# Kernel tuning notes

Hardware: AMD Instinct MI355X
Metric: run time of the kernel (lower is better)

## Reference

```python
import jax, jax.numpy as jnp
import numpy as np

B, C, H, W = 32, 1024, 32, 32  # N = H*W must equal C for the attn_c * attn_s broadcast
C8 = C // 8


def setup_inputs() -> dict:
    key = jax.random.key(0)
    ks = jax.random.split(key, 9)
    s = 1.0 / np.sqrt(C)
    return {
        "z": jax.random.normal(ks[0], (B, C, H, W), jnp.float32),
        "x": jax.random.normal(ks[1], (B, C, H, W), jnp.float32),
        "y": jax.random.normal(ks[2], (B, C, H, W), jnp.float32),
        "Wq": jax.random.normal(ks[3], (C8, C), jnp.float32) * s,
        "bq": jax.random.normal(ks[4], (C8,), jnp.float32) * 0.01,
        "Wk": jax.random.normal(ks[5], (C8, C), jnp.float32) * s,
        "bk": jax.random.normal(ks[6], (C8,), jnp.float32) * 0.01,
        "Wv": jax.random.normal(ks[7], (C, C), jnp.float32) * s,
        "bv": jax.random.normal(ks[8], (C,), jnp.float32) * 0.01,
    }


def reference(z, x, y, Wq, bq, Wk, bk, Wv, bv):
    b, c, h, w = x.shape
    n = h * w
    xf = x.reshape(b, c, n)
    yf = y.reshape(b, c, n)
    zf = z.reshape(b, c, n)

    # 1x1 convs == channel matmuls
    q = jnp.einsum('oc,bcn->bon', Wq, xf) + bq[None, :, None]   # (B, C/8, N)
    k = jnp.einsum('oc,bcn->bon', Wk, yf) + bk[None, :, None]   # (B, C/8, N)

    # channel-projected spatial attention: (B, N, N)
    energy_c = jnp.einsum('bcn,bcm->bnm', q, k)
    attention_c = jax.nn.softmax(energy_c, axis=-1)

    # raw channel attention: (B, C, C)
    energy_s = jnp.einsum('bcn,bdn->bcd', xf, yf)
    energy_s = jnp.max(energy_s, axis=-1, keepdims=True) - energy_s
    attention_s = jax.nn.softmax(energy_s, axis=-1)

    # multiplicative combine + third softmax (requires N == C)
    attention = jax.nn.softmax(attention_c * attention_s, axis=-1)

    v = jnp.einsum('oc,bcn->bon', Wv, zf) + bv[None, :, None]   # (B, C, N)
    # out[b,c,m] = sum_n v[b,c,n] * attention[b,m,n]  (value @ attention^T)
    out = jnp.einsum('bcn,bmn->bcm', v, attention)
    return z + out.reshape(b, c, h, w)
```

## Files before the change

kernel.cpp:

```cpp
#include <hip/hip_runtime.h>
#include <hip/hip_bf16.h>

typedef __attribute__((ext_vector_type(8))) short s8_t;
typedef __attribute__((ext_vector_type(4))) float f4_t;

__device__ __forceinline__ unsigned short f2bf(float f) {
  union { float f; unsigned u; } x; x.f = f;
  unsigned r = x.u + 0x7fffu + ((x.u >> 16) & 1u);
  return (unsigned short)(r >> 16);
}

__device__ __forceinline__ void split2(float e0, float e1, unsigned& hp, unsigned& lp) {
  unsigned b0 = __float_as_uint(e0), b1 = __float_as_uint(e1);
  unsigned h0 = b0 & 0xFFFF0000u, h1 = b1 & 0xFFFF0000u;
  hp = (b0 >> 16) | h1;
  float l0 = e0 - __uint_as_float(h0), l1 = e1 - __uint_as_float(h1);
  lp = (__float_as_uint(l0) >> 16) | (__float_as_uint(l1) & 0xFFFF0000u);
}

__device__ __forceinline__ void gload16(const void* g, void* l) {
  __builtin_amdgcn_global_load_lds(
      (const __attribute__((address_space(1))) void*)g,
      (__attribute__((address_space(3))) void*)l, 16, 0, 0);
}

__device__ __forceinline__ void swz_grid(int& bx, int& by, int& bz) {
  const int gx = gridDim.x, gy = gridDim.y;
  const int nwg = gx * gy * gridDim.z;
  const int flat = (blockIdx.z * gy + blockIdx.y) * gx + blockIdx.x;
  const int s = (flat & 7) * (nwg >> 3) + (flat >> 3);
  bx = s % gx;
  const int r = s / gx;
  by = r % gy;
  bz = r / gy;
}

__global__ __launch_bounds__(256) void k_convert(const float* __restrict__ in,
                                                 unsigned short* __restrict__ out, int n) {
  int i = (blockIdx.x * 256 + threadIdx.x) * 8;
  if (i >= n) return;
  float4 a = *(const float4*)(in + i);
  float4 b = *(const float4*)(in + i + 4);
  ushort4 u0; u0.x = f2bf(a.x); u0.y = f2bf(a.y); u0.z = f2bf(a.z); u0.w = f2bf(a.w);
  ushort4 u1; u1.x = f2bf(b.x); u1.y = f2bf(b.y); u1.z = f2bf(b.z); u1.w = f2bf(b.w);
  *(ushort4*)(out + i) = u0;
  *(ushort4*)(out + i + 4) = u1;
}

__global__ __launch_bounds__(256) void k_transp32(const float* __restrict__ in,
                                                  float* __restrict__ out) {
  __shared__ float tile[64][65];
  const int t = threadIdx.x, b = blockIdx.z;
  const int r0 = blockIdx.y * 64, c0 = blockIdx.x * 64;
  const float* ip = in + (size_t)b * 1048576;
  float* op = out + (size_t)b * 1048576;
  const int tr = t >> 4, tc = (t & 15) * 4;
#pragma unroll
  for (int p = 0; p < 4; ++p) {
    int r = p * 16 + tr;
    float4 v = *(const float4*)(ip + (size_t)(r0 + r) * 1024 + c0 + tc);
    tile[r][tc] = v.x; tile[r][tc + 1] = v.y; tile[r][tc + 2] = v.z; tile[r][tc + 3] = v.w;
  }
  __syncthreads();
#pragma unroll
  for (int p = 0; p < 4; ++p) {
    int n = p * 16 + tr;
    float4 w;
    w.x = tile[tc][n]; w.y = tile[tc + 1][n]; w.z = tile[tc + 2][n]; w.w = tile[tc + 3][n];
    *(float4*)(op + (size_t)(c0 + n) * 1024 + r0 + tc) = w;
  }
}

__global__ __launch_bounds__(256) void k_transpbf(const float* __restrict__ in,
                                                  unsigned short* __restrict__ outt) {
  __shared__ unsigned short tile[64][72];
  const int t = threadIdx.x, b = blockIdx.z;
  const int r0 = blockIdx.y * 64, c0 = blockIdx.x * 64;
  const float* ip = in + (size_t)b * 1048576;
  const int tr = t >> 4, tc = (t & 15) * 4;
#pragma unroll
  for (int p = 0; p < 4; ++p) {
    int r = p * 16 + tr;
    float4 v = *(const float4*)(ip + (size_t)(r0 + r) * 1024 + c0 + tc);
    tile[r][tc] = f2bf(v.x); tile[r][tc + 1] = f2bf(v.y);
    tile[r][tc + 2] = f2bf(v.z); tile[r][tc + 3] = f2bf(v.w);
  }
  __syncthreads();
#pragma unroll
  for (int p = 0; p < 4; ++p) {
    int n = p * 16 + tr;
    ushort4 w;
    w.x = tile[tc][n]; w.y = tile[tc + 1][n]; w.z = tile[tc + 2][n]; w.w = tile[tc + 3][n];
    *(ushort4*)(outt + (size_t)b * 1048576 + (size_t)(c0 + n) * 1024 + r0 + tc) = w;
  }
}

__device__ __forceinline__ void split_write(unsigned short* buf, int wbase,
                                            const float* av, const float* bv) {
  unsigned ah[8], al[8], bh[8], bl[8];
#pragma unroll
  for (int p = 0; p < 8; ++p) {
    split2(av[2 * p], av[2 * p + 1], ah[p], al[p]);
    split2(bv[2 * p], bv[2 * p + 1], bh[p], bl[p]);
  }
  *(uint4*)(buf + wbase) = *(uint4*)(ah);
  *(uint4*)(buf + wbase + 8) = *(uint4*)(ah + 4);
  *(uint4*)(buf + 4096 + wbase) = *(uint4*)(al);
  *(uint4*)(buf + 4096 + wbase + 8) = *(uint4*)(al + 4);
  *(uint4*)(buf + 8192 + wbase) = *(uint4*)(bh);
  *(uint4*)(buf + 8192 + wbase + 8) = *(uint4*)(bh + 4);
  *(uint4*)(buf + 12288 + wbase) = *(uint4*)(bl);
  *(uint4*)(buf + 12288 + wbase + 8) = *(uint4*)(bl + 4);
}

template <int BIAS_MODE>
__global__ __launch_bounds__(256) void k_mfma3(
    const float* __restrict__ A, int lda, long long sA,
    const float* __restrict__ B, int ldb, long long sB,
    float* __restrict__ C, int ldc, long long sC,
    const float* __restrict__ bias, int K) {
  __shared__ __align__(16) unsigned short sm[16384];
  const int tid = threadIdx.x;
  const int lane = tid & 63, wave = tid >> 6;
  const int wr = wave >> 1, wc = wave & 1;
  const int bz = blockIdx.z;
  const int m0 = blockIdx.x * 128, n0 = blockIdx.y * 128;

  const int sr = tid >> 1, sh = (tid & 1) * 16;
  const float* ag = A + (long long)bz * sA + (long long)(m0 + sr) * lda + sh;
  const float* bg = B + (long long)bz * sB + (long long)(n0 + sr) * ldb + sh;
  const int wbase = sr * 32 + sh;

  const int lr = lane & 15, lg = lane >> 4;
  const int fa = (wr * 64 + lr) * 32 + lg * 8;
  const int fb = (wc * 64 + lr) * 32 + lg * 8;

  f4_t acc[4][4];
#pragma unroll
  for (int i = 0; i < 4; ++i)
#pragma unroll
    for (int j = 0; j < 4; ++j) acc[i][j] = (f4_t)0.f;

  for (int k0 = 0; k0 < K; k0 += 32) {
    float av[16], bv[16];
#pragma unroll
    for (int p = 0; p < 4; ++p) {
      *(float4*)(av + p * 4) = *(const float4*)(ag + p * 4);
      *(float4*)(bv + p * 4) = *(const float4*)(bg + p * 4);
    }
    split_write(sm, wbase, av, bv);
    ag += 32; bg += 32;
    __syncthreads();
    const unsigned short* Ahp = sm;
    const unsigned short* Alp = sm + 4096;
    const unsigned short* Bhp = sm + 8192;
    const unsigned short* Blp = sm + 12288;
    s8_t fah[4], fbh[4], ftmp[4];
#pragma unroll
    for (int f = 0; f < 4; ++f) {
      fah[f] = *(const s8_t*)(Ahp + fa + f * 512);
      fbh[f] = *(const s8_t*)(Bhp + fb + f * 512);
    }
#pragma unroll
    for (int i = 0; i < 4; ++i)
#pragma unroll
      for (int j = 0; j < 4; ++j)
        acc[i][j] = __builtin_amdgcn_mfma_f32_16x16x32_bf16(fah[i], fbh[j], acc[i][j], 0, 0, 0);
#pragma unroll
    for (int f = 0; f < 4; ++f) ftmp[f] = *(const s8_t*)(Blp + fb + f * 512);
#pragma unroll
    for (int i = 0; i < 4; ++i)
#pragma unroll
      for (int j = 0; j < 4; ++j)
        acc[i][j] = __builtin_amdgcn_mfma_f32_16x16x32_bf16(fah[i], ftmp[j], acc[i][j], 0, 0, 0);
#pragma unroll
    for (int f = 0; f < 4; ++f) ftmp[f] = *(const s8_t*)(Alp + fa + f * 512);
#pragma unroll
    for (int i = 0; i < 4; ++i)
#pragma unroll
      for (int j = 0; j < 4; ++j)
        acc[i][j] = __builtin_amdgcn_mfma_f32_16x16x32_bf16(ftmp[i], fbh[j], acc[i][j], 0, 0, 0);
    __syncthreads();
  }

#pragma unroll
  for (int i = 0; i < 4; ++i) {
    const int rbase = m0 + wr * 64 + i * 16 + lg * 4;
#pragma unroll
    for (int j = 0; j < 4; ++j) {
      const int col = n0 + wc * 64 + j * 16 + lr;
      float bc = (BIAS_MODE == 2) ? bias[col] : 0.f;
#pragma unroll
      for (int e = 0; e < 4; ++e) {
        float v = acc[i][j][e];
        if (BIAS_MODE == 2) v += bc;
        C[(long long)bz * sC + (long long)(rbase + e) * ldc + col] = v;
      }
    }
  }
}

template <int BIAS_MODE, bool OUT_BF16, bool RESID>
__global__ __launch_bounds__(256) void k_mfma(
    const unsigned short* __restrict__ A, int lda, long long sA,
    const unsigned short* __restrict__ B, int ldb, long long sB,
    void* __restrict__ Cp, int ldc, long long sC,
    const float* __restrict__ bias,
    const float* __restrict__ resid, long long sR, int K) {
  __shared__ __align__(16) unsigned short As[8192];
  __shared__ __align__(16) unsigned short Bs[8192];
  int bxs, bys, bz; swz_grid(bxs, bys, bz);
  const int tid = threadIdx.x;
  const int lane = tid & 63, wave = tid >> 6;
  const int wr = wave >> 1, wc = wave & 1;
  const int m0 = bxs * 128, n0 = bys * 128;

  const int ch0 = wave * 64 + lane, ch1 = ch0 + 256;
  const unsigned short* pa0 = A + (long long)bz * sA + (long long)(m0 + (ch0 >> 2)) * lda + (ch0 & 3) * 8;
  const unsigned short* pa1 = A + (long long)bz * sA + (long long)(m0 + (ch1 >> 2)) * lda + (ch1 & 3) * 8;
  const unsigned short* pb0 = B + (long long)bz * sB + (long long)(n0 + (ch0 >> 2)) * ldb + (ch0 & 3) * 8;
  const unsigned short* pb1 = B + (long long)bz * sB + (long long)(n0 + (ch1 >> 2)) * ldb + (ch1 & 3) * 8;

  const int lr = lane & 15, lg = lane >> 4;
  const int fa = (wr * 64 + lr) * 32 + lg * 8;
  const int fb = (wc * 64 + lr) * 32 + lg * 8;

  f4_t acc[4][4];
#pragma unroll
  for (int i = 0; i < 4; ++i)
#pragma unroll
    for (int j = 0; j < 4; ++j) acc[i][j] = (f4_t)0.f;

  const int nt = K >> 5;
  int cur = 0;

  auto stage = [&](int b) {
    char* la = (char*)As + b * 8192 + wave * 1024;
    char* lb = (char*)Bs + b * 8192 + wave * 1024;
    gload16(pa0, la); gload16(pa1, la + 4096);
    gload16(pb0, lb); gload16(pb1, lb + 4096);
    pa0 += 32; pa1 += 32; pb0 += 32; pb1 += 32;
  };

  stage(0);
  asm volatile("s_waitcnt vmcnt(0)" ::: "memory");
  __builtin_amdgcn_s_barrier();

  for (int t = 0; t < nt; ++t) {
    const bool more = (t + 1 < nt);
    if (more) stage(cur ^ 1);
    const unsigned short* ap = As + cur * 4096;
    const unsigned short* bp = Bs + cur * 4096;
    s8_t af[4], bf[4];
#pragma unroll
    for (int f = 0; f < 4; ++f) {
      af[f] = *(const s8_t*)(ap + fa + f * 512);
      bf[f] = *(const s8_t*)(bp + fb + f * 512);
    }
#pragma unroll
    for (int i = 0; i < 4; ++i)
#pragma unroll
      for (int j = 0; j < 4; ++j)
        acc[i][j] = __builtin_amdgcn_mfma_f32_16x16x32_bf16(af[i], bf[j], acc[i][j], 0, 0, 0);
    if (more) {
      asm volatile("s_waitcnt vmcnt(0)" ::: "memory");
      __builtin_amdgcn_s_barrier();
    }
    cur ^= 1;
  }

#pragma unroll
  for (int i = 0; i < 4; ++i) {
    const int rbase = m0 + wr * 64 + i * 16 + lg * 4;
#pragma unroll
    for (int j = 0; j < 4; ++j) {
      const int col = n0 + wc * 64 + j * 16 + lr;
#pragma unroll
      for (int e = 0; e < 4; ++e) {
        const int row = rbase + e;
        float v = acc[i][j][e];
        if (BIAS_MODE == 1) v += bias[row];
        const long long off = (long long)bz * sC + (long long)row * ldc + col;
        if (RESID) v += resid[(long long)bz * sR + (long long)row * ldc + col];
        if (OUT_BF16) ((unsigned short*)Cp)[off] = f2bf(v);
        else          ((float*)Cp)[off] = v;
      }
    }
  }
}

__device__ __forceinline__ float wave_red_max(float v) {
#pragma unroll
  for (int o = 32; o > 0; o >>= 1) v = fmaxf(v, __shfl_down(v, o, 64));
  return v;
}
__device__ __forceinline__ float wave_red_sum(float v) {
#pragma unroll
  for (int o = 32; o > 0; o >>= 1) v += __shfl_down(v, o, 64);
  return v;
}
__device__ __forceinline__ float block_red_max(float v, float* red) {
  v = wave_red_max(v);
  if ((threadIdx.x & 63) == 0) red[threadIdx.x >> 6] = v;
  __syncthreads();
  v = fmaxf(fmaxf(red[0], red[1]), fmaxf(red[2], red[3]));
  __syncthreads();
  return v;
}
__device__ __forceinline__ float block_red_sum(float v, float* red) {
  v = wave_red_sum(v);
  if ((threadIdx.x & 63) == 0) red[threadIdx.x >> 6] = v;
  __syncthreads();
  v = red[0] + red[1] + red[2] + red[3];
  __syncthreads();
  return v;
}

__global__ __launch_bounds__(256) void k_combine(float* __restrict__ ec,
                                                 const float* __restrict__ es) {
  __shared__ float red[4];
  const size_t row = blockIdx.x;
  float* cp = ec + row * 1024;
  const float* sp = es + row * 1024;
  const int tid = threadIdx.x;
  float4 c4 = ((const float4*)cp)[tid];
  float4 s4 = ((const float4*)sp)[tid];

  float mx = fmaxf(fmaxf(c4.x, c4.y), fmaxf(c4.z, c4.w));
  mx = block_red_max(mx, red);
  float e0 = __expf(c4.x - mx), e1 = __expf(c4.y - mx);
  float e2 = __expf(c4.z - mx), e3 = __expf(c4.w - mx);
  float sc = block_red_sum(e0 + e1 + e2 + e3, red);

  float t0 = -s4.x, t1 = -s4.y, t2 = -s4.z, t3 = -s4.w;
  float mt = fmaxf(fmaxf(t0, t1), fmaxf(t2, t3));
  mt = block_red_max(mt, red);
  float f0 = __expf(t0 - mt), f1 = __expf(t1 - mt);
  float f2 = __expf(t2 - mt), f3 = __expf(t3 - mt);
  float ss = block_red_sum(f0 + f1 + f2 + f3, red);

  const float rc = 1.f / sc, rs = 1.f / ss;
  float g0 = __expf((e0 * rc) * (f0 * rs));
  float g1 = __expf((e1 * rc) * (f1 * rs));
  float g2 = __expf((e2 * rc) * (f2 * rs));
  float g3 = __expf((e3 * rc) * (f3 * rs));
  float s3 = block_red_sum(g0 + g1 + g2 + g3, red);
  const float r3 = 1.f / s3;
  ushort4 o;
  o.x = f2bf(g0 * r3); o.y = f2bf(g1 * r3); o.z = f2bf(g2 * r3); o.w = f2bf(g3 * r3);
  ((ushort4*)cp)[tid] = o;
}

extern "C" void kernel_launch(void* const* d_in, const int* in_sizes, int n_in,
                              void* d_out, int out_size, void* d_ws, size_t ws_size,
                              hipStream_t stream) {
  const float* z = (const float*)d_in[0];
  const float* x = (const float*)d_in[1];
  const float* y = (const float*)d_in[2];
  const float* Wq = (const float*)d_in[3];
  const float* bq = (const float*)d_in[4];
  const float* Wk = (const float*)d_in[5];
  const float* bk = (const float*)d_in[6];
  const float* Wv = (const float*)d_in[7];
  const float* bv = (const float*)d_in[8];
  float* out = (float*)d_out;

  char* ws = (char*)d_ws;
  float* es = (float*)ws;
  unsigned short* z_t = (unsigned short*)ws;
  unsigned short* v_bf = z_t + 33554432;
  char* wsB = ws + 134217728;
  float* xytf = (float*)wsB;
  float* ec = (float*)wsB;
  unsigned short* attn = (unsigned short*)wsB;
  char* wsC = ws + 268435456;
  float* q_t = (float*)wsC;
  float* k_t = q_t + 4194304;
  unsigned short* wv = (unsigned short*)wsC;

  dim3 blk(256);
  hipLaunchKernelGGL(k_transp32, dim3(16, 16, 32), blk, 0, stream, x, xytf);
  hipLaunchKernelGGL((k_mfma3<2>), dim3(8, 1, 32), blk, 0, stream,
                     xytf, 1024, 1048576LL, Wq, 1024, 0LL, q_t, 128, 131072LL, bq, 1024);
  hipLaunchKernelGGL(k_transp32, dim3(16, 16, 32), blk, 0, stream, y, xytf);
  hipLaunchKernelGGL((k_mfma3<2>), dim3(8, 1, 32), blk, 0, stream,
                     xytf, 1024, 1048576LL, Wk, 1024, 0LL, k_t, 128, 131072LL, bk, 1024);
  hipLaunchKernelGGL((k_mfma3<0>), dim3(8, 8, 32), blk, 0, stream,
                     x, 1024, 1048576LL, y, 1024, 1048576LL, es, 1024, 1048576LL,
                     (const float*)nullptr, 1024);
  hipLaunchKernelGGL((k_mfma3<0>), dim3(8, 8, 32), blk, 0, stream,
                     q_t, 128, 131072LL, k_t, 128, 131072LL, ec, 1024, 1048576LL,
                     (const float*)nullptr, 128);
  hipLaunchKernelGGL(k_combine, dim3(32768), blk, 0, stream, ec, es);
  hipLaunchKernelGGL(k_transpbf, dim3(16, 16, 32), blk, 0, stream, z, z_t);
  hipLaunchKernelGGL(k_convert, dim3(512), blk, 0, stream, Wv, wv, 1048576);
  hipLaunchKernelGGL((k_mfma<1, true, false>), dim3(8, 8, 32), blk, 0, stream,
                     wv, 1024, 0LL, z_t, 1024, 1048576LL, (void*)v_bf, 1024, 1048576LL,
                     bv, (const float*)nullptr, 0LL, 1024);
  hipLaunchKernelGGL((k_mfma<0, false, true>), dim3(8, 8, 32), blk, 0, stream,
                     v_bf, 1024, 1048576LL, attn, 2048, 2097152LL, (void*)out, 1024, 1048576LL,
                     (const float*)nullptr, z, 1048576LL, 1024);
}
```

Measured before the change: 877.3 us.

## Triple-buffer LDS staging in bf16 MFMA GEMM and swizzle fp32 GEMM grid

Replaces the double-buffered global-to-LDS loads in the bf16 MFMA GEMM with a three-stage ring buffer. Two tiles are prefetched ahead, and partial vmcnt waits let loads overlap with the current tile's MFMAs. A second barrier after compute protects the slot being reused. The fp32 split GEMM kernel also adopts the swizzled block mapping for better cache locality. In exchange, LDS use grows by half per block, which may reduce occupancy, and each iteration now has two barriers.

Result: no change. 866.2 us (-1.3%).

```diff
diff --git a/kernel.cpp b/kernel.cpp
--- a/kernel.cpp
+++ b/kernel.cpp
@@ -120,11 +120,11 @@
     float* __restrict__ C, int ldc, long long sC,
     const float* __restrict__ bias, int K) {
   __shared__ __align__(16) unsigned short sm[16384];
+  int bxs, bys, bz; swz_grid(bxs, bys, bz);
   const int tid = threadIdx.x;
   const int lane = tid & 63, wave = tid >> 6;
   const int wr = wave >> 1, wc = wave & 1;
-  const int bz = blockIdx.z;
-  const int m0 = blockIdx.x * 128, n0 = blockIdx.y * 128;
+  const int m0 = bxs * 128, n0 = bys * 128;
 
   const int sr = tid >> 1, sh = (tid & 1) * 16;
   const float* ag = A + (long long)bz * sA + (long long)(m0 + sr) * lda + sh;
@@ -207,8 +207,8 @@
     void* __restrict__ Cp, int ldc, long long sC,
     const float* __restrict__ bias,
     const float* __restrict__ resid, long long sR, int K) {
-  __shared__ __align__(16) unsigned short As[8192];
-  __shared__ __align__(16) unsigned short Bs[8192];
+  __shared__ __align__(16) unsigned short As[12288];
+  __shared__ __align__(16) unsigned short Bs[12288];
   int bxs, bys, bz; swz_grid(bxs, bys, bz);
   const int tid = threadIdx.x;
   const int lane = tid & 63, wave = tid >> 6;
@@ -231,26 +231,35 @@
 #pragma unroll
     for (int j = 0; j < 4; ++j) acc[i][j] = (f4_t)0.f;
 
-  const int nt = K >> 5;
-  int cur = 0;
-
-  auto stage = [&](int b) {
-    char* la = (char*)As + b * 8192 + wave * 1024;
-    char* lb = (char*)Bs + b * 8192 + wave * 1024;
-    gload16(pa0, la); gload16(pa1, la + 4096);
-    gload16(pb0, lb); gload16(pb1, lb + 4096);
+  char* a0 = (char*)As; char* a1 = a0 + 8192; char* a2 = a0 + 16384;
+  char* b0 = (char*)Bs; char* b1 = b0 + 8192; char* b2 = b0 + 16384;
+
+  auto stage = [&](char* la, char* lb) {
+    gload16(pa0, la + wave * 1024);
+    gload16(pa1, la + 4096 + wave * 1024);
+    gload16(pb0, lb + wave * 1024);
+    gload16(pb1, lb + 4096 + wave * 1024);
     pa0 += 32; pa1 += 32; pb0 += 32; pb1 += 32;
   };
 
-  stage(0);
-  asm volatile("s_waitcnt vmcnt(0)" ::: "memory");
-  __builtin_amdgcn_s_barrier();
+  const int nt = K >> 5;
+  stage(a0, b0);
+  stage(a1, b1);
 
   for (int t = 0; t < nt; ++t) {
-    const bool more = (t + 1 < nt);
-    if (more) stage(cur ^ 1);
-    const unsigned short* ap = As + cur * 4096;
-    const unsigned short* bp = Bs + cur * 4096;
+    if (t + 2 < nt) {
+      stage(a2, b2);
+      asm volatile("s_waitcnt vmcnt(8)" ::: "memory");
+    } else if (t + 1 < nt) {
+      asm volatile("s_waitcnt vmcnt(4)" ::: "memory");
+    } else {
+      asm volatile("s_waitcnt vmcnt(0)" ::: "memory");
+    }
+    __builtin_amdgcn_sched_barrier(0);
+    __builtin_amdgcn_s_barrier();
+    __builtin_amdgcn_sched_barrier(0);
+    const unsigned short* ap = (const unsigned short*)a0;
+    const unsigned short* bp = (const unsigned short*)b0;
     s8_t af[4], bf[4];
 #pragma unroll
     for (int f = 0; f < 4; ++f) {
@@ -262,11 +271,11 @@
 #pragma unroll
       for (int j = 0; j < 4; ++j)
         acc[i][j] = __builtin_amdgcn_mfma_f32_16x16x32_bf16(af[i], bf[j], acc[i][j], 0, 0, 0);
-    if (more) {
-      asm volatile("s_waitcnt vmcnt(0)" ::: "memory");
-      __builtin_amdgcn_s_barrier();
-    }
-    cur ^= 1;
+    __builtin_amdgcn_sched_barrier(0);
+    __builtin_amdgcn_s_barrier();
+    __builtin_amdgcn_sched_barrier(0);
+    char* ta = a0; a0 = a1; a1 = a2; a2 = ta;
+    char* tb = b0; b0 = b1; b1 = b2; b2 = tb;
   }
 
 #pragma unroll
```
